# Kernel optimization log

Measured on AMD Instinct MI355X. Metric: run time of the kernel, lower is better.

## Reference

```python
import jax, jax.numpy as jnp
import numpy as np

N = 65536          # total atoms
M = 12             # max neighbors
ORIG = 92          # orig_atom_fea_len
NBR = 41           # nbr_fea_len
AF = 64            # atom_fea_len
NCONV = 3
HF = 128           # h_fea_len
N0 = 1024          # number of crystals
EPS = 1e-5


def _glorot(key, shape):
    fan_in, fan_out = shape[0], shape[-1]
    lim = np.sqrt(6.0 / (fan_in + fan_out)).astype(np.float32)
    return jax.random.uniform(key, shape, jnp.float32, -lim, lim)


def setup_inputs() -> dict:
    key = jax.random.key(0)
    ks = jax.random.split(key, 16)
    atom_fea = jax.random.normal(ks[0], (N, ORIG), jnp.float32)
    nbr_fea = jax.random.normal(ks[1], (N, M, NBR), jnp.float32)
    nbr_fea_idx = jax.random.randint(ks[2], (N, M), 0, N, jnp.int32)
    # flat segment ids: ~64 atoms per crystal, contiguous (mimics ragged idx lists)
    crystal_idx = jnp.repeat(jnp.arange(N0, dtype=jnp.int32), N // N0)
    # parameters
    emb_w = _glorot(ks[3], (ORIG, AF)); emb_b = jnp.zeros((AF,), jnp.float32)
    conv_fc_w = _glorot(ks[4], (NCONV, 2 * AF + NBR, 2 * AF))
    conv_fc_b = jnp.zeros((NCONV, 2 * AF), jnp.float32)
    conv_bn1_g = jnp.ones((NCONV, 2 * AF), jnp.float32)
    conv_bn1_b = jnp.zeros((NCONV, 2 * AF), jnp.float32)
    conv_bn2_g = jnp.ones((NCONV, AF), jnp.float32)
    conv_bn2_b = jnp.zeros((NCONV, AF), jnp.float32)
    fc1_w = _glorot(ks[5], (AF, HF)); fc1_b = jnp.zeros((HF,), jnp.float32)
    out1_w = _glorot(ks[6], (HF, HF // 2)); out1_b = jnp.zeros((HF // 2,), jnp.float32)
    out2_w = _glorot(ks[7], (HF // 2, 1)); out2_b = jnp.zeros((1,), jnp.float32)
    return dict(atom_fea=atom_fea, nbr_fea=nbr_fea, nbr_fea_idx=nbr_fea_idx,
                crystal_idx=crystal_idx, emb_w=emb_w, emb_b=emb_b,
                conv_fc_w=conv_fc_w, conv_fc_b=conv_fc_b,
                conv_bn1_g=conv_bn1_g, conv_bn1_b=conv_bn1_b,
                conv_bn2_g=conv_bn2_g, conv_bn2_b=conv_bn2_b,
                fc1_w=fc1_w, fc1_b=fc1_b, out1_w=out1_w, out1_b=out1_b,
                out2_w=out2_w, out2_b=out2_b)


def _batchnorm(x, g, b):
    # training-mode BatchNorm1d over axis 0, biased variance, eps=1e-5
    mu = jnp.mean(x, axis=0)
    var = jnp.var(x, axis=0)
    return (x - mu) * jax.lax.rsqrt(var + EPS) * g + b


def _conv_layer(afea, nbr_fea, nbr_idx, w, b, g1, b1, g2, b2):
    # gather neighbor atom features: (N, M, AF)
    atom_nbr = afea[nbr_idx]
    self_fea = jnp.broadcast_to(afea[:, None, :], (N, M, AF))
    total = jnp.concatenate([self_fea, atom_nbr, nbr_fea], axis=-1)  # (N, M, 2AF+NBR)
    gated = jnp.einsum('nmf,fg->nmg', total, w) + b                  # (N, M, 2AF)
    gated = _batchnorm(gated.reshape(-1, 2 * AF), g1, b1).reshape(N, M, 2 * AF)
    filt, core = jnp.split(gated, 2, axis=-1)
    nbr_sumed = jnp.sum(jax.nn.sigmoid(filt) * jax.nn.softplus(core), axis=1)  # scatter-sum over nbrs
    nbr_sumed = _batchnorm(nbr_sumed, g2, b2)
    return jax.nn.softplus(afea + nbr_sumed)


def reference(atom_fea, nbr_fea, nbr_fea_idx, crystal_idx, emb_w, emb_b,
              conv_fc_w, conv_fc_b, conv_bn1_g, conv_bn1_b, conv_bn2_g, conv_bn2_b,
              fc1_w, fc1_b, out1_w, out1_b, out2_w, out2_b):
    afea = atom_fea @ emb_w + emb_b                 # (N, AF)
    identity = afea
    for i in range(NCONV):
        afea = _conv_layer(afea, nbr_fea, nbr_fea_idx,
                           conv_fc_w[i], conv_fc_b[i],
                           conv_bn1_g[i], conv_bn1_b[i],
                           conv_bn2_g[i], conv_bn2_b[i])
        afea = afea + identity
        identity = afea
    # ragged per-crystal mean pooling via segment_sum
    sums = jax.ops.segment_sum(afea, crystal_idx, num_segments=N0)
    counts = jax.ops.segment_sum(jnp.ones((N,), afea.dtype), crystal_idx, num_segments=N0)
    crys = sums / jnp.maximum(counts, 1.0)[:, None]  # (N0, AF)
    crys = jax.nn.softplus(crys) @ fc1_w + fc1_b
    crys = jax.nn.softplus(crys)                     # (N0, HF) == repr
    out = jax.nn.softplus(crys @ out1_w + out1_b) @ out2_w + out2_b  # (N0, 1)
    return out, crys
```

## Files before the change

### kernel.cpp

```cpp
#include <hip/hip_runtime.h>

#define NATOM 65536
#define MNBR 12
#define NMROW (NATOM*MNBR)
#define ORIG 92
#define NBRF 41
#define AF 64
#define HF 128
#define NCRYS 1024
#define NTILES (NMROW/96)
#define EPSBN 1e-5f
#define NBP 48
#define CGRID 2048

typedef __attribute__((ext_vector_type(8))) short short8;
typedef __attribute__((ext_vector_type(4))) float floatx4;

__device__ __forceinline__ float softplusf_(float x){
    return fmaxf(x,0.f) + __logf(1.f + __expf(-fabsf(x)));
}
__device__ __forceinline__ float sigmoidf_(float x){
    return __builtin_amdgcn_rcpf(1.f + __expf(-x));
}
__device__ __forceinline__ short f2bf(float x){
    unsigned u = __float_as_uint(x);
    u += 0x7fffu + ((u >> 16) & 1u);
    return (short)(u >> 16);
}

__global__ void k_embed(const float* __restrict__ atom_fea, const float* __restrict__ emb_w,
                        const float* __restrict__ emb_b, float* __restrict__ afea,
                        short* __restrict__ abf)
{
    __shared__ float wl[ORIG*AF];
    __shared__ float bl[AF];
    __shared__ float rows[4*ORIG];
    int tid = threadIdx.x;
    for (int i = tid; i < ORIG*AF; i += 256) wl[i] = emb_w[i];
    if (tid < AF) bl[tid] = emb_b[tid];
    __syncthreads();
    for (int t = blockIdx.x; t < NATOM/4; t += gridDim.x) {
        for (int i = tid; i < 4*ORIG; i += 256) rows[i] = atom_fea[t*4*ORIG + i];
        __syncthreads();
        int r = tid >> 6, c = tid & 63;
        float acc = bl[c];
        const float* rp = &rows[r*ORIG];
        #pragma unroll 4
        for (int k = 0; k < ORIG; ++k) acc += rp[k] * wl[k*AF + c];
        int n = t*4 + r;
        afea[n*AF + c] = acc;
        abf[n*AF + c] = f2bf(acc);
        __syncthreads();
    }
}

__global__ void k_prep_nbr(const float* __restrict__ nbr_fea, short* __restrict__ nbf)
{
    int g = blockIdx.x*256 + threadIdx.x;
    int row = g / NBP, k = g % NBP;
    float v = (k < NBRF) ? nbr_fea[row*NBRF + k] : 0.f;
    nbf[g] = f2bf(v);
}

__global__ void k_prep_w(const float* __restrict__ W, short* __restrict__ wt2)
{
    int g = blockIdx.x*256 + threadIdx.x;
    int j = g & 7, c = (g >> 3) & 127, q = (g >> 10) & 3, ks = g >> 12;
    int k = ks*32 + q*8 + j;
    wt2[g] = (k < 169) ? f2bf(W[k*128 + c]) : (short)0;
}

template<int PASS2>
__global__ __launch_bounds__(256, 4)
void k_conv(const short* __restrict__ abf, const short* __restrict__ nbf,
            const int* __restrict__ nbr_idx, const short* __restrict__ wt2,
            const float* __restrict__ bias,
            float* __restrict__ stats1, const float* __restrict__ bn1ss,
            float* __restrict__ nsum, float* __restrict__ stats2)
{
    __shared__ __align__(16) short stg[6144];
    __shared__ float pbuf[4*12*17];

    int tid = threadIdx.x;
    int lane = tid & 63, wave = tid >> 6;
    int l15 = lane & 15, q = lane >> 4;
    int cf = wave*16 + l15;
    int cc = 64 + cf;

    short8 wf[6][2];
    #pragma unroll
    for (int ks = 0; ks < 6; ++ks) {
        wf[ks][0] = *(const short8*)(wt2 + ((ks*4+q)*128 + cf)*8);
        wf[ks][1] = *(const short8*)(wt2 + ((ks*4+q)*128 + cc)*8);
    }
    float bs0 = bias[cf], bs1 = bias[cc];
    float sc0=0.f, sh0=0.f, sc1=0.f, sh1=0.f;
    if (PASS2) { sc0=bn1ss[cf]; sh0=bn1ss[128+cf]; sc1=bn1ss[cc]; sh1=bn1ss[128+cc]; }

    float s_acc[2]={0.f,0.f}, s2_acc[2]={0.f,0.f};
    float st2s = 0.f, st2q = 0.f;
    const short8 zf = {0,0,0,0,0,0,0,0};
    float* pb = pbuf + wave*(12*17);

    for (int bt = blockIdx.x; bt < NTILES*2; bt += CGRID) {
        int tile = bt >> 1, rh = bt & 1;
        int R0 = tile*96 + rh*48;

        __syncthreads();
        #pragma unroll
        for (int it = 0; it < 3; ++it) {
            int i = tid + it*256;
            if (i < 384) {
                int row = i >> 3, c = i & 7;
                int j = nbr_idx[R0 + row];
                *(short8*)(stg + row*72 + c*8) = *(const short8*)(abf + (unsigned)j*64u + c*8);
            } else if (i < 672) {
                int j2 = i - 384;
                int row = j2 / 6, c = j2 % 6;
                *(short8*)(stg + 3456 + row*56 + c*8) =
                    *(const short8*)(nbf + (unsigned)(R0 + row)*48u + c*8);
            }
        }
        short8 sv[3][2];
        #pragma unroll
        for (int rt = 0; rt < 3; ++rt) {
            const short* sp = abf + (unsigned)((R0 + rt*16 + l15)/12u)*64u + q*8;
            sv[rt][0] = *(const short8*)sp;
            sv[rt][1] = *(const short8*)(sp + 32);
        }
        __syncthreads();

        floatx4 acc[3][2];
        #pragma unroll
        for (int rt=0; rt<3; ++rt) {
            acc[rt][0] = (floatx4){bs0,bs0,bs0,bs0};
            acc[rt][1] = (floatx4){bs1,bs1,bs1,bs1};
        }

        #pragma unroll
        for (int rt = 0; rt < 3; ++rt) {
            int r = rt*16 + l15;
            short8 nv0 = *(const short8*)(stg + r*72 + q*8);
            short8 nv1 = *(const short8*)(stg + r*72 + 32 + q*8);
            short8 ev0 = *(const short8*)(stg + 3456 + r*56 + q*8);
            short8 ev1 = (q < 2) ? *(const short8*)(stg + 3456 + r*56 + 32 + q*8) : zf;
            #pragma unroll
            for (int ct = 0; ct < 2; ++ct) {
                acc[rt][ct] = __builtin_amdgcn_mfma_f32_16x16x32_bf16(sv[rt][0], wf[0][ct], acc[rt][ct], 0,0,0);
                acc[rt][ct] = __builtin_amdgcn_mfma_f32_16x16x32_bf16(sv[rt][1], wf[1][ct], acc[rt][ct], 0,0,0);
                acc[rt][ct] = __builtin_amdgcn_mfma_f32_16x16x32_bf16(nv0,      wf[2][ct], acc[rt][ct], 0,0,0);
                acc[rt][ct] = __builtin_amdgcn_mfma_f32_16x16x32_bf16(nv1,      wf[3][ct], acc[rt][ct], 0,0,0);
                acc[rt][ct] = __builtin_amdgcn_mfma_f32_16x16x32_bf16(ev0,      wf[4][ct], acc[rt][ct], 0,0,0);
                acc[rt][ct] = __builtin_amdgcn_mfma_f32_16x16x32_bf16(ev1,      wf[5][ct], acc[rt][ct], 0,0,0);
            }
        }

        if (!PASS2) {
            #pragma unroll
            for (int ct=0; ct<2; ++ct)
                #pragma unroll
                for (int rt=0; rt<3; ++rt)
                    #pragma unroll
                    for (int r=0; r<4; ++r) {
                        float v = acc[rt][ct][r];
                        s_acc[ct] += v; s2_acc[ct] += v*v;
                    }
        } else {
            #pragma unroll
            for (int rt=0; rt<3; ++rt) {
                float part = 0.f;
                #pragma unroll
                for (int r=0; r<4; ++r) {
                    float f = acc[rt][0][r]*sc0 + sh0;
                    float g = acc[rt][1][r]*sc1 + sh1;
                    part += sigmoidf_(f) * softplusf_(g);
                }
                pb[(rt*4+q)*17 + l15] = part;
            }
            int a = lane >> 4, c16 = lane & 15;
            float s = pb[(3*a+0)*17 + c16] + pb[(3*a+1)*17 + c16] + pb[(3*a+2)*17 + c16];
            nsum[(tile*8 + rh*4 + a)*AF + wave*16 + c16] = s;
            st2s += s; st2q += s*s;
        }
    }

    if (!PASS2) {
        #pragma unroll
        for (int ct=0; ct<2; ++ct) {
            float s = s_acc[ct], s2 = s2_acc[ct];
            s  += __shfl_xor(s, 16);  s  += __shfl_xor(s, 32);
            s2 += __shfl_xor(s2, 16); s2 += __shfl_xor(s2, 32);
            if (q == 0) {
                int c = ct ? cc : cf;
                atomicAdd(&stats1[c], s);
                atomicAdd(&stats1[128 + c], s2);
            }
        }
    } else {
        st2s += __shfl_xor(st2s, 16); st2s += __shfl_xor(st2s, 32);
        st2q += __shfl_xor(st2q, 16); st2q += __shfl_xor(st2q, 32);
        if (q == 0) {
            atomicAdd(&stats2[cf], st2s);
            atomicAdd(&stats2[64 + cf], st2q);
        }
    }
}

__global__ void k_bn1fin(const float* __restrict__ stats1, const float* __restrict__ g,
                         const float* __restrict__ b, float* __restrict__ bn1ss)
{
    int c = threadIdx.x;
    float mean = stats1[c] * (1.f/NMROW);
    float var  = stats1[128+c] * (1.f/NMROW) - mean*mean;
    float scale = g[c] * rsqrtf(var + EPSBN);
    bn1ss[c] = scale;
    bn1ss[128+c] = b[c] - mean*scale;
}

__global__ void k_update(float* __restrict__ afea, short* __restrict__ abf,
                         const float* __restrict__ nsum,
                         const float* __restrict__ stats2,
                         const float* __restrict__ g2, const float* __restrict__ b2)
{
    int g = blockIdx.x*256 + threadIdx.x;
    int c = g & 63;
    float mean = stats2[c] * (1.f/NATOM);
    float var  = stats2[64+c] * (1.f/NATOM) - mean*mean;
    float scale = g2[c]*rsqrtf(var + EPSBN);
    float shift = b2[c] - mean*scale;
    float ns = nsum[g]*scale + shift;
    float a = afea[g];
    float v = softplusf_(a + ns) + a;
    afea[g] = v; abf[g] = f2bf(v);
}

__global__ void k_pool(const float* __restrict__ afea, const int* __restrict__ cidx,
                       float* __restrict__ pool, float* __restrict__ cnt)
{
    int g = blockIdx.x*256 + threadIdx.x;
    int c = g & 63; int chunk = g >> 6;
    float run = 0.f, rc = 0.f; int cur = -1;
    for (int i = 0; i < 16; ++i) {
        int a = chunk*16 + i;
        int cr = cidx[a];
        float v = afea[a*64 + c];
        if (cr != cur) {
            if (cur >= 0) { atomicAdd(&pool[cur*64+c], run); if (c==0) atomicAdd(&cnt[cur], rc); }
            run = 0.f; rc = 0.f; cur = cr;
        }
        run += v; rc += 1.f;
    }
    atomicAdd(&pool[cur*64+c], run); if (c==0) atomicAdd(&cnt[cur], rc);
}

__global__ void k_head(const float* __restrict__ pool, const float* __restrict__ cnt,
                       const float* __restrict__ fc1w, const float* __restrict__ fc1b,
                       const float* __restrict__ o1w, const float* __restrict__ o1b,
                       const float* __restrict__ o2w, const float* __restrict__ o2b,
                       float* __restrict__ dout)
{
    __shared__ float spv[64], crys[128], h1[64];
    int b = blockIdx.x, tid = threadIdx.x;
    if (tid < 64) {
        float ct = fmaxf(cnt[b], 1.f);
        spv[tid] = softplusf_(pool[b*64+tid] / ct);
    }
    __syncthreads();
    float a = fc1b[tid];
    for (int k = 0; k < 64; ++k) a += spv[k] * fc1w[k*128 + tid];
    float v = softplusf_(a);
    crys[tid] = v;
    dout[NCRYS + b*128 + tid] = v;
    __syncthreads();
    if (tid < 64) {
        float a2 = o1b[tid];
        for (int k = 0; k < 128; ++k) a2 += crys[k] * o1w[k*64 + tid];
        h1[tid] = softplusf_(a2) * o2w[tid];
    }
    __syncthreads();
    if (tid == 0) {
        float s = o2b[0];
        for (int j = 0; j < 64; ++j) s += h1[j];
        dout[b] = s;
    }
}

extern "C" void kernel_launch(void* const* d_in, const int* in_sizes, int n_in,
                              void* d_out, int out_size, void* d_ws, size_t ws_size,
                              hipStream_t stream)
{
    const float* atom_fea = (const float*)d_in[0];
    const float* nbr_fea  = (const float*)d_in[1];
    const int*   nbr_idx  = (const int*)d_in[2];
    const int*   cidx     = (const int*)d_in[3];
    const float* emb_w    = (const float*)d_in[4];
    const float* emb_b    = (const float*)d_in[5];
    const float* cfw      = (const float*)d_in[6];
    const float* cfb      = (const float*)d_in[7];
    const float* bn1g     = (const float*)d_in[8];
    const float* bn1b     = (const float*)d_in[9];
    const float* bn2g     = (const float*)d_in[10];
    const float* bn2b     = (const float*)d_in[11];
    const float* fc1w     = (const float*)d_in[12];
    const float* fc1b     = (const float*)d_in[13];
    const float* o1w      = (const float*)d_in[14];
    const float* o1b      = (const float*)d_in[15];
    const float* o2w      = (const float*)d_in[16];
    const float* o2b      = (const float*)d_in[17];

    float* ws    = (float*)d_ws;
    float* afea  = ws;
    float* nsum  = ws + 4194304;
    short* abf   = (short*)(ws + 8388608);
    short* nbf   = (short*)(ws + 10485760);
    short* wt2   = (short*)(ws + 29360128);
    float* stats = ws + 29372416;
    float* pool  = ws + 29374336;
    float* cnt   = ws + 29439872;

    hipMemsetAsync(stats, 0, (1920 + 65536 + 1024)*sizeof(float), stream);

    k_prep_nbr<<<(NMROW*NBP)/256, 256, 0, stream>>>(nbr_fea, nbf);
    k_embed<<<2048, 256, 0, stream>>>(atom_fea, emb_w, emb_b, afea, abf);

    for (int L = 0; L < 3; ++L) {
        float* st1 = stats + L*640;
        float* ss  = st1 + 256;
        float* st2 = st1 + 512;
        k_prep_w<<<96, 256, 0, stream>>>(cfw + L*169*128, wt2);
        k_conv<0><<<CGRID, 256, 0, stream>>>(abf, nbf, nbr_idx, wt2, cfb + L*128, st1, nullptr, nullptr, nullptr);
        k_bn1fin<<<1, 128, 0, stream>>>(st1, bn1g + L*128, bn1b + L*128, ss);
        k_conv<1><<<CGRID, 256, 0, stream>>>(abf, nbf, nbr_idx, wt2, cfb + L*128, nullptr, ss, nsum, st2);
        k_update<<<16384, 256, 0, stream>>>(afea, abf, nsum, st2, bn2g + L*64, bn2b + L*64);
    }
    k_pool<<<1024, 256, 0, stream>>>(afea, cidx, pool, cnt);
    k_head<<<NCRYS, 128, 0, stream>>>(pool, cnt, fc1w, fc1b, o1w, o1b, o2w, o2b, (float*)d_out);
}
```

Baseline: 963.4 us.

## Double-buffer LDS staging in conv kernel with register-held prefetch of next tile

Restructures the conv kernel's tile loop into a fixed 8-iteration software pipeline. Gathered neighbor features, edge features and self-atom features for the next 48-row task are prefetched into registers, with neighbor indices fetched two tasks ahead, while MFMA runs on the current LDS buffer. The self-atom rows now also go through LDS instead of per-lane global loads. This aims to hide global gather latency, at the cost of twice the LDS, more registers and launch bounds lowered from 4 to 3 blocks per CU.

Measured after the change: 849.7 us. 1.13x faster.

```diff
diff --git a/kernel.cpp b/kernel.cpp
--- a/kernel.cpp
+++ b/kernel.cpp
@@ -8,10 +8,10 @@
 #define AF 64
 #define HF 128
 #define NCRYS 1024
-#define NTILES (NMROW/96)
 #define EPSBN 1e-5f
 #define NBP 48
 #define CGRID 2048
+#define NTASK 16384
 
 typedef __attribute__((ext_vector_type(8))) short short8;
 typedef __attribute__((ext_vector_type(4))) float floatx4;
@@ -71,14 +71,14 @@
 }
 
 template<int PASS2>
-__global__ __launch_bounds__(256, 4)
+__global__ __launch_bounds__(256, 3)
 void k_conv(const short* __restrict__ abf, const short* __restrict__ nbf,
             const int* __restrict__ nbr_idx, const short* __restrict__ wt2,
             const float* __restrict__ bias,
             float* __restrict__ stats1, const float* __restrict__ bn1ss,
             float* __restrict__ nsum, float* __restrict__ stats2)
 {
-    __shared__ __align__(16) short stg[6144];
+    __shared__ __align__(16) short stg[2][6432];
     __shared__ float pbuf[4*12*17];
 
     int tid = threadIdx.x;
@@ -97,61 +97,91 @@
     float sc0=0.f, sh0=0.f, sc1=0.f, sh1=0.f;
     if (PASS2) { sc0=bn1ss[cf]; sh0=bn1ss[128+cf]; sc1=bn1ss[cc]; sh1=bn1ss[128+cc]; }
 
+    int kind[3], ldso[3], nrow[3]; long gco[3];
+    #pragma unroll
+    for (int s = 0; s < 3; ++s) {
+        int i = tid + s*256;
+        if (i < 384)      { kind[s]=0; int row=i>>3, c=i&7; nrow[s]=row; ldso[s]=row*72+c*8; gco[s]=c*8; }
+        else if (i < 672) { kind[s]=1; int j=i-384; int row=j/6, c=j%6; nrow[s]=0; ldso[s]=3456+row*56+c*8; gco[s]=row*48+c*8; }
+        else if (i < 704) { kind[s]=2; int j=i-672; int a=j>>3, c=j&7; nrow[s]=0; ldso[s]=6144+a*72+c*8; gco[s]=a*64+c*8; }
+        else              { kind[s]=3; nrow[s]=0; ldso[s]=0; gco[s]=0; }
+    }
+    int art[3], nvo[3], evo[3], svo[3];
+    #pragma unroll
+    for (int rt = 0; rt < 3; ++rt) {
+        int r = rt*16 + l15;
+        art[rt] = r/12;
+        nvo[rt] = r*72 + q*8;
+        evo[rt] = 3456 + r*56 + q*8;
+        svo[rt] = 6144 + art[rt]*72 + q*8;
+    }
+
     float s_acc[2]={0.f,0.f}, s2_acc[2]={0.f,0.f};
     float st2s = 0.f, st2q = 0.f;
     const short8 zf = {0,0,0,0,0,0,0,0};
     float* pb = pbuf + wave*(12*17);
-
-    for (int bt = blockIdx.x; bt < NTILES*2; bt += CGRID) {
-        int tile = bt >> 1, rh = bt & 1;
-        int R0 = tile*96 + rh*48;
-
-        __syncthreads();
-        #pragma unroll
-        for (int it = 0; it < 3; ++it) {
-            int i = tid + it*256;
-            if (i < 384) {
-                int row = i >> 3, c = i & 7;
-                int j = nbr_idx[R0 + row];
-                *(short8*)(stg + row*72 + c*8) = *(const short8*)(abf + (unsigned)j*64u + c*8);
-            } else if (i < 672) {
-                int j2 = i - 384;
-                int row = j2 / 6, c = j2 % 6;
-                *(short8*)(stg + 3456 + row*56 + c*8) =
-                    *(const short8*)(nbf + (unsigned)(R0 + row)*48u + c*8);
-            }
-        }
-        short8 sv[3][2];
-        #pragma unroll
-        for (int rt = 0; rt < 3; ++rt) {
-            const short* sp = abf + (unsigned)((R0 + rt*16 + l15)/12u)*64u + q*8;
-            sv[rt][0] = *(const short8*)sp;
-            sv[rt][1] = *(const short8*)(sp + 32);
-        }
-        __syncthreads();
-
+    const int bt = blockIdx.x;
+
+    int nid[3];
+    short8 hold[3];
+    #pragma unroll
+    for (int s = 0; s < 3; ++s)
+        if (kind[s]==0) nid[s] = nbr_idx[bt*48 + nrow[s]];
+    #pragma unroll
+    for (int s = 0; s < 3; ++s) {
+        if (kind[s]==0)      hold[s] = *(const short8*)(abf + (unsigned)nid[s]*64u + gco[s]);
+        else if (kind[s]==1) hold[s] = *(const short8*)(nbf + (long)bt*2304 + gco[s]);
+        else if (kind[s]==2) hold[s] = *(const short8*)(abf + (unsigned)bt*256u + gco[s]);
+    }
+    #pragma unroll
+    for (int s = 0; s < 3; ++s)
+        if (kind[s]==0) nid[s] = nbr_idx[(bt+CGRID)*48 + nrow[s]];
+    #pragma unroll
+    for (int s = 0; s < 3; ++s)
+        if (kind[s] < 3) *(short8*)(&stg[0][0] + ldso[s]) = hold[s];
+    __syncthreads();
+
+    #pragma unroll 2
+    for (int k = 0; k < 8; ++k) {
+        int b = bt + k*CGRID;
+        if (k < 7) {
+            int bn = b + CGRID;
+            #pragma unroll
+            for (int s = 0; s < 3; ++s) {
+                if (kind[s]==0)      hold[s] = *(const short8*)(abf + (unsigned)nid[s]*64u + gco[s]);
+                else if (kind[s]==1) hold[s] = *(const short8*)(nbf + (long)bn*2304 + gco[s]);
+                else if (kind[s]==2) hold[s] = *(const short8*)(abf + (unsigned)bn*256u + gco[s]);
+            }
+            if (k < 6) {
+                #pragma unroll
+                for (int s = 0; s < 3; ++s)
+                    if (kind[s]==0) nid[s] = nbr_idx[(bn+CGRID)*48 + nrow[s]];
+            }
+        }
+
+        const short* sb = &stg[k & 1][0];
         floatx4 acc[3][2];
         #pragma unroll
         for (int rt=0; rt<3; ++rt) {
             acc[rt][0] = (floatx4){bs0,bs0,bs0,bs0};
             acc[rt][1] = (floatx4){bs1,bs1,bs1,bs1};
         }
-
         #pragma unroll
         for (int rt = 0; rt < 3; ++rt) {
-            int r = rt*16 + l15;
-            short8 nv0 = *(const short8*)(stg + r*72 + q*8);
-            short8 nv1 = *(const short8*)(stg + r*72 + 32 + q*8);
-            short8 ev0 = *(const short8*)(stg + 3456 + r*56 + q*8);
-            short8 ev1 = (q < 2) ? *(const short8*)(stg + 3456 + r*56 + 32 + q*8) : zf;
+            short8 sv0 = *(const short8*)(sb + svo[rt]);
+            short8 sv1 = *(const short8*)(sb + svo[rt] + 32);
+            short8 nv0 = *(const short8*)(sb + nvo[rt]);
+            short8 nv1 = *(const short8*)(sb + nvo[rt] + 32);
+            short8 ev0 = *(const short8*)(sb + evo[rt]);
+            short8 ev1 = (q < 2) ? *(const short8*)(sb + evo[rt] + 32) : zf;
             #pragma unroll
             for (int ct = 0; ct < 2; ++ct) {
-                acc[rt][ct] = __builtin_amdgcn_mfma_f32_16x16x32_bf16(sv[rt][0], wf[0][ct], acc[rt][ct], 0,0,0);
-                acc[rt][ct] = __builtin_amdgcn_mfma_f32_16x16x32_bf16(sv[rt][1], wf[1][ct], acc[rt][ct], 0,0,0);
-                acc[rt][ct] = __builtin_amdgcn_mfma_f32_16x16x32_bf16(nv0,      wf[2][ct], acc[rt][ct], 0,0,0);
-                acc[rt][ct] = __builtin_amdgcn_mfma_f32_16x16x32_bf16(nv1,      wf[3][ct], acc[rt][ct], 0,0,0);
-                acc[rt][ct] = __builtin_amdgcn_mfma_f32_16x16x32_bf16(ev0,      wf[4][ct], acc[rt][ct], 0,0,0);
-                acc[rt][ct] = __builtin_amdgcn_mfma_f32_16x16x32_bf16(ev1,      wf[5][ct], acc[rt][ct], 0,0,0);
+                acc[rt][ct] = __builtin_amdgcn_mfma_f32_16x16x32_bf16(sv0, wf[0][ct], acc[rt][ct], 0,0,0);
+                acc[rt][ct] = __builtin_amdgcn_mfma_f32_16x16x32_bf16(sv1, wf[1][ct], acc[rt][ct], 0,0,0);
+                acc[rt][ct] = __builtin_amdgcn_mfma_f32_16x16x32_bf16(nv0, wf[2][ct], acc[rt][ct], 0,0,0);
+                acc[rt][ct] = __builtin_amdgcn_mfma_f32_16x16x32_bf16(nv1, wf[3][ct], acc[rt][ct], 0,0,0);
+                acc[rt][ct] = __builtin_amdgcn_mfma_f32_16x16x32_bf16(ev0, wf[4][ct], acc[rt][ct], 0,0,0);
+                acc[rt][ct] = __builtin_amdgcn_mfma_f32_16x16x32_bf16(ev1, wf[5][ct], acc[rt][ct], 0,0,0);
             }
         }
 
@@ -179,9 +209,17 @@
             }
             int a = lane >> 4, c16 = lane & 15;
             float s = pb[(3*a+0)*17 + c16] + pb[(3*a+1)*17 + c16] + pb[(3*a+2)*17 + c16];
-            nsum[(tile*8 + rh*4 + a)*AF + wave*16 + c16] = s;
+            nsum[(b*4 + a)*AF + wave*16 + c16] = s;
             st2s += s; st2q += s*s;
         }
+
+        if (k < 7) {
+            short* db = &stg[(k + 1) & 1][0];
+            #pragma unroll
+            for (int s = 0; s < 3; ++s)
+                if (kind[s] < 3) *(short8*)(db + ldso[s]) = hold[s];
+        }
+        __syncthreads();
     }
 
     if (!PASS2) {
```
